# Performance work log

Hardware: AMD Instinct MI355X
Metric: run time of the kernel (lower is better)

## Reference

```python
import jax, jax.numpy as jnp
import numpy as np


def setup_inputs() -> dict:
    key = jax.random.key(0)
    k0, k1, k2, k3, k4 = jax.random.split(key, 5)
    feat0 = jax.random.normal(k0, (32, 256, 56, 56), dtype=jnp.float32)
    feat1 = jax.random.normal(k1, (32, 512, 28, 28), dtype=jnp.float32)
    feat2 = jax.random.normal(k2, (32, 1024, 14, 14), dtype=jnp.float32)
    feat3 = jax.random.normal(k3, (32, 2048, 7, 7), dtype=jnp.float32)
    # Conv2d(3840 -> 1024, kernel_size=1, bias=False): weight [emb, C_total]
    conv_w = jax.random.normal(k4, (1024, 3840), dtype=jnp.float32) * 0.02
    return {"feat0": feat0, "feat1": feat1, "feat2": feat2, "feat3": feat3, "conv_w": conv_w}


def reference(feat0, feat1, feat2, feat3, conv_w):
    # Target spatial size = earliest (largest) level.
    Ht, Wt = feat0.shape[2], feat0.shape[3]

    def up_mean(f):
        # Bilinear upsample (torch Upsample align_corners=False == jax 'bilinear'
        # half-pixel resize), then spatial mean per channel.  Because the 1x1
        # conv and global avg-pool are linear, pooling each upsampled level
        # first and applying the conv on the pooled vector is exactly the
        # same math as conv(concat(upsampled)) followed by avg-pool.
        B, C = f.shape[0], f.shape[1]
        up = jax.image.resize(f, (B, C, Ht, Wt), method='bilinear')  # [B,C,Ht,Wt]
        return jnp.mean(up, axis=(2, 3))  # [B,C]

    v = jnp.concatenate([up_mean(f) for f in (feat0, feat1, feat2, feat3)], axis=1)  # [B, 3840]
    # 1x1 conv (no bias) on pooled vector == GEMM with conv weight, then squeeze.
    return v @ conv_w.T  # [B, emb]
```

## Files before the change

### kernel.cpp

```cpp
#include <hip/hip_runtime.h>


__global__ __launch_bounds__(256) void pool_kernel(
    const float* __restrict__ f0, const float* __restrict__ f1,
    const float* __restrict__ f2, const float* __restrict__ f3,
    float* __restrict__ v)
{
    __shared__ float l[3136];
    int bid = blockIdx.x;
    int t = threadIdx.x;

    if (bid < 8192) {
        const float4* p = (const float4*)(f0 + (size_t)bid * 3136);
        float4 a = p[t], b2 = p[t + 256], c = p[t + 512];
        float s = a.x + a.y + a.z + a.w
                + b2.x + b2.y + b2.z + b2.w
                + c.x + c.y + c.z + c.w;
        if (t < 16) { float4 d = p[t + 768]; s += d.x + d.y + d.z + d.w; }
        #pragma unroll
        for (int o = 32; o; o >>= 1) s += __shfl_xor(s, o);
        if ((t & 63) == 0) l[t >> 6] = s;
        __syncthreads();
        if (t == 0)
            v[(bid >> 8) * 3840 + (bid & 255)] =
                (l[0] + l[1] + l[2] + l[3]) * (1.f / 3136.f);
        return;
    }

    float4* lf = (float4*)l;
    if (bid < 12288) {
        int blk = bid - 8192;
        const float4* src = (const float4*)(f1 + (size_t)blk * 3136);
        lf[t] = src[t]; lf[t + 256] = src[t + 256]; lf[t + 512] = src[t + 512];
        if (t < 16) lf[t + 768] = src[t + 768];
        __syncthreads();
        int w = t >> 6, lane = t & 63;
        const float* base = l + w * 784;
        float s = 0.f;
        #pragma unroll
        for (int i = 0; i < 12; ++i) s += base[lane + (i << 6)];
        if (lane < 16) s += base[768 + lane];
        #pragma unroll
        for (int o = 32; o; o >>= 1) s += __shfl_xor(s, o);
        if (lane == 0) {
            int q = blk * 4 + w;
            v[(q >> 9) * 3840 + 256 + (q & 511)] = s * (1.f / 784.f);
        }
    } else if (bid < 14336) {
        int blk = bid - 12288;
        const float4* src = (const float4*)(f2 + (size_t)blk * 3136);
        lf[t] = src[t]; lf[t + 256] = src[t + 256]; lf[t + 512] = src[t + 512];
        if (t < 16) lf[t + 768] = src[t + 768];
        __syncthreads();
        int p = t >> 4, j = t & 15;
        const float* base = l + p * 196;
        float s = 0.f;
        #pragma unroll
        for (int i = 0; i < 12; ++i) s += base[j + (i << 4)];
        if (j < 4) s += base[192 + j];
        s += __shfl_xor(s, 8); s += __shfl_xor(s, 4);
        s += __shfl_xor(s, 2); s += __shfl_xor(s, 1);
        if (j == 0) {
            int q = blk * 16 + p;
            v[(q >> 10) * 3840 + 768 + (q & 1023)] = s * (1.f / 196.f);
        }
    } else {
        int blk = bid - 14336;
        const float4* src = (const float4*)(f3 + (size_t)blk * 3136);
        lf[t] = src[t]; lf[t + 256] = src[t + 256]; lf[t + 512] = src[t + 512];
        if (t < 16) lf[t + 768] = src[t + 768];
        __syncthreads();
        int p = t >> 2, j = t & 3;
        const float* base = l + p * 49;
        float s = 0.f;
        #pragma unroll
        for (int i = 0; i < 12; ++i) s += base[j + (i << 2)];
        if (j == 0) s += base[48];
        s += __shfl_xor(s, 2); s += __shfl_xor(s, 1);
        if (j == 0) {
            int q = blk * 64 + p;
            v[(q >> 11) * 3840 + 1792 + (q & 2047)] = s * (1.f / 49.f);
        }
    }
}

#define KT 120

__global__ __launch_bounds__(256) void gemm_kernel(
    const float* __restrict__ v, const float* __restrict__ W,
    float* __restrict__ partials)
{
    __shared__ float vs[32][124];
    __shared__ float wsh[64][124];
    int t = threadIdx.x;
    int et = blockIdx.x & 15, ks = blockIdx.x >> 4;
    int e0 = et << 6, k0 = ks * KT;

    {
        int f = t;
        #pragma unroll
        for (int i = 0; i < 3; ++i, f += 256) {
            int row = f / 30, c4 = f % 30;
            *(float4*)&vs[row][c4 * 4] =
                *(const float4*)&v[row * 3840 + k0 + c4 * 4];
        }
        if (t < 192) {
            f = t + 768;
            int row = f / 30, c4 = f % 30;
            *(float4*)&vs[row][c4 * 4] =
                *(const float4*)&v[row * 3840 + k0 + c4 * 4];
        }
    }
    {
        int f = t;
        #pragma unroll
        for (int i = 0; i < 7; ++i, f += 256) {
            int row = f / 30, c4 = f % 30;
            *(float4*)&wsh[row][c4 * 4] =
                *(const float4*)&W[(size_t)(e0 + row) * 3840 + k0 + c4 * 4];
        }
        if (t < 128) {
            f = t + 1792;
            int row = f / 30, c4 = f % 30;
            *(float4*)&wsh[row][c4 * 4] =
                *(const float4*)&W[(size_t)(e0 + row) * 3840 + k0 + c4 * 4];
        }
    }
    __syncthreads();

    int bg = t >> 5, eg = t & 31;
    int b0 = bg << 2;
    float acc[4][2] = {};
    #pragma unroll 5
    for (int k = 0; k < KT; k += 4) {
        float4 vv[4], ww[2];
        #pragma unroll
        for (int i = 0; i < 4; ++i) vv[i] = *(const float4*)&vs[b0 + i][k];
        #pragma unroll
        for (int j = 0; j < 2; ++j) ww[j] = *(const float4*)&wsh[eg + (j << 5)][k];
        #pragma unroll
        for (int i = 0; i < 4; ++i)
            #pragma unroll
            for (int j = 0; j < 2; ++j)
                acc[i][j] += vv[i].x * ww[j].x + vv[i].y * ww[j].y +
                             vv[i].z * ww[j].z + vv[i].w * ww[j].w;
    }

    float* pout = partials + (size_t)ks * 32768 + (size_t)b0 * 1024 + e0 + eg;
    #pragma unroll
    for (int i = 0; i < 4; ++i)
        #pragma unroll
        for (int j = 0; j < 2; ++j)
            pout[i * 1024 + (j << 5)] = acc[i][j];
}

__global__ __launch_bounds__(256) void reduce_kernel(
    const float* __restrict__ partials, float* __restrict__ out)
{
    int idx = blockIdx.x * 256 + threadIdx.x;
    float s = 0.f;
    #pragma unroll
    for (int sp = 0; sp < 32; ++sp) s += partials[sp * 32768 + idx];
    out[idx] = s;
}

extern "C" void kernel_launch(void* const* d_in, const int* in_sizes, int n_in,
                              void* d_out, int out_size, void* d_ws, size_t ws_size,
                              hipStream_t stream)
{
    const float* f0 = (const float*)d_in[0];
    const float* f1 = (const float*)d_in[1];
    const float* f2 = (const float*)d_in[2];
    const float* f3 = (const float*)d_in[3];
    const float* W  = (const float*)d_in[4];
    float* out = (float*)d_out;

    float* v        = (float*)d_ws;
    float* partials = v + 32 * 3840;

    pool_kernel<<<15360, 256, 0, stream>>>(f0, f1, f2, f3, v);
    gemm_kernel<<<512, 256, 0, stream>>>(v, W, partials);
    reduce_kernel<<<128, 256, 0, stream>>>(partials, out);
}
```

Before: 233.7 us.

## Use direct global-to-LDS loads with larger pool blocks and unified segment sums

Rewrites the pooling kernel so each block loads 4 channel-groups of 3136 floats straight into LDS via global_load_lds. Every thread then sums one 49-element segment, followed by level-specific shuffle reductions. This cuts the grid from 15360 to 3840 blocks and avoids staging through registers. The GEMM staging now issues all global loads before the shared stores, and the reduce kernel uses four independent accumulators. The 50KB LDS footprint limits occupancy and may reduce memory-level parallelism.

```diff
diff --git a/kernel.cpp b/kernel.cpp
--- a/kernel.cpp
+++ b/kernel.cpp
@@ -1,86 +1,68 @@
 #include <hip/hip_runtime.h>
 
+
+#define AS1(p) ((const __attribute__((address_space(1))) void*)(p))
+#define AS3(p) ((__attribute__((address_space(3))) void*)(p))
 
 __global__ __launch_bounds__(256) void pool_kernel(
     const float* __restrict__ f0, const float* __restrict__ f1,
     const float* __restrict__ f2, const float* __restrict__ f3,
     float* __restrict__ v)
 {
-    __shared__ float l[3136];
-    int bid = blockIdx.x;
-    int t = threadIdx.x;
+    __shared__ float l[12544];
+    int bid = blockIdx.x, t = threadIdx.x;
+    int wave = t >> 6, lane = t & 63;
 
-    if (bid < 8192) {
-        const float4* p = (const float4*)(f0 + (size_t)bid * 3136);
-        float4 a = p[t], b2 = p[t + 256], c = p[t + 512];
-        float s = a.x + a.y + a.z + a.w
-                + b2.x + b2.y + b2.z + b2.w
-                + c.x + c.y + c.z + c.w;
-        if (t < 16) { float4 d = p[t + 768]; s += d.x + d.y + d.z + d.w; }
+    const float* base;
+    if (bid < 2048)      base = f0 + (size_t)bid * 12544;
+    else if (bid < 3072) base = f1 + (size_t)(bid - 2048) * 12544;
+    else if (bid < 3584) base = f2 + (size_t)(bid - 3072) * 12544;
+    else                 base = f3 + (size_t)(bid - 3584) * 12544;
+
+    {
+        const float* g = base + wave * 3136;
+        float* ld = l + wave * 3136;
         #pragma unroll
-        for (int o = 32; o; o >>= 1) s += __shfl_xor(s, o);
-        if ((t & 63) == 0) l[t >> 6] = s;
-        __syncthreads();
-        if (t == 0)
-            v[(bid >> 8) * 3840 + (bid & 255)] =
-                (l[0] + l[1] + l[2] + l[3]) * (1.f / 3136.f);
-        return;
+        for (int r = 0; r < 12; ++r) {
+            __builtin_amdgcn_global_load_lds(
+                AS1(g + r * 256 + lane * 4), AS3(ld + r * 256), 16, 0, 0);
+        }
+        if (lane < 16) {
+            __builtin_amdgcn_global_load_lds(
+                AS1(g + 3072 + lane * 4), AS3(ld + 3072), 16, 0, 0);
+        }
     }
+    asm volatile("s_waitcnt vmcnt(0)" ::: "memory");
+    __syncthreads();
 
-    float4* lf = (float4*)l;
-    if (bid < 12288) {
-        int blk = bid - 8192;
-        const float4* src = (const float4*)(f1 + (size_t)blk * 3136);
-        lf[t] = src[t]; lf[t + 256] = src[t + 256]; lf[t + 512] = src[t + 512];
-        if (t < 16) lf[t + 768] = src[t + 768];
-        __syncthreads();
-        int w = t >> 6, lane = t & 63;
-        const float* base = l + w * 784;
-        float s = 0.f;
-        #pragma unroll
-        for (int i = 0; i < 12; ++i) s += base[lane + (i << 6)];
-        if (lane < 16) s += base[768 + lane];
+    const float* seg = l + t * 49;
+    float s = 0.f;
+    #pragma unroll
+    for (int i = 0; i < 49; ++i) s += seg[i];
+
+    if (bid < 2048) {
         #pragma unroll
         for (int o = 32; o; o >>= 1) s += __shfl_xor(s, o);
         if (lane == 0) {
-            int q = blk * 4 + w;
+            int q = bid * 4 + wave;
+            v[(q >> 8) * 3840 + (q & 255)] = s * (1.f / 3136.f);
+        }
+    } else if (bid < 3072) {
+        s += __shfl_xor(s, 8); s += __shfl_xor(s, 4);
+        s += __shfl_xor(s, 2); s += __shfl_xor(s, 1);
+        if ((t & 15) == 0) {
+            int q = (bid - 2048) * 16 + (t >> 4);
             v[(q >> 9) * 3840 + 256 + (q & 511)] = s * (1.f / 784.f);
         }
-    } else if (bid < 14336) {
-        int blk = bid - 12288;
-        const float4* src = (const float4*)(f2 + (size_t)blk * 3136);
-        lf[t] = src[t]; lf[t + 256] = src[t + 256]; lf[t + 512] = src[t + 512];
-        if (t < 16) lf[t + 768] = src[t + 768];
-        __syncthreads();
-        int p = t >> 4, j = t & 15;
-        const float* base = l + p * 196;
-        float s = 0.f;
-        #pragma unroll
-        for (int i = 0; i < 12; ++i) s += base[j + (i << 4)];
-        if (j < 4) s += base[192 + j];
-        s += __shfl_xor(s, 8); s += __shfl_xor(s, 4);
+    } else if (bid < 3584) {
         s += __shfl_xor(s, 2); s += __shfl_xor(s, 1);
-        if (j == 0) {
-            int q = blk * 16 + p;
+        if ((t & 3) == 0) {
+            int q = (bid - 3072) * 64 + (t >> 2);
             v[(q >> 10) * 3840 + 768 + (q & 1023)] = s * (1.f / 196.f);
         }
     } else {
-        int blk = bid - 14336;
-        const float4* src = (const float4*)(f3 + (size_t)blk * 3136);
-        lf[t] = src[t]; lf[t + 256] = src[t + 256]; lf[t + 512] = src[t + 512];
-        if (t < 16) lf[t + 768] = src[t + 768];
-        __syncthreads();
-        int p = t >> 2, j = t & 3;
-        const float* base = l + p * 49;
-        float s = 0.f;
-        #pragma unroll
-        for (int i = 0; i < 12; ++i) s += base[j + (i << 2)];
-        if (j == 0) s += base[48];
-        s += __shfl_xor(s, 2); s += __shfl_xor(s, 1);
-        if (j == 0) {
-            int q = blk * 64 + p;
-            v[(q >> 11) * 3840 + 1792 + (q & 2047)] = s * (1.f / 49.f);
-        }
+        int q = (bid - 3584) * 256 + t;
+        v[(q >> 11) * 3840 + 1792 + (q & 2047)] = s * (1.f / 49.f);
     }
 }
 
@@ -97,34 +79,46 @@
     int e0 = et << 6, k0 = ks * KT;
 
     {
-        int f = t;
+        float4 tmp[7];
+        int row[7], c4[7];
         #pragma unroll
-        for (int i = 0; i < 3; ++i, f += 256) {
-            int row = f / 30, c4 = f % 30;
-            *(float4*)&vs[row][c4 * 4] =
-                *(const float4*)&v[row * 3840 + k0 + c4 * 4];
+        for (int i = 0; i < 7; ++i) {
+            int f = t + (i << 8);
+            row[i] = f / 30; c4[i] = f % 30;
+            tmp[i] = *(const float4*)&W[(size_t)(e0 + row[i]) * 3840 + k0 + c4[i] * 4];
         }
-        if (t < 192) {
-            f = t + 768;
-            int row = f / 30, c4 = f % 30;
-            *(float4*)&vs[row][c4 * 4] =
-                *(const float4*)&v[row * 3840 + k0 + c4 * 4];
+        float4 tail; int rowt = 0, c4t = 0;
+        if (t < 128) {
+            int f = t + 1792;
+            rowt = f / 30; c4t = f % 30;
+            tail = *(const float4*)&W[(size_t)(e0 + rowt) * 3840 + k0 + c4t * 4];
         }
+        #pragma unroll
+        for (int i = 0; i < 7; ++i)
+            *(float4*)&wsh[row[i]][c4[i] * 4] = tmp[i];
+        if (t < 128)
+            *(float4*)&wsh[rowt][c4t * 4] = tail;
     }
     {
-        int f = t;
+        float4 tmp[3];
+        int row[3], c4[3];
         #pragma unroll
-        for (int i = 0; i < 7; ++i, f += 256) {
-            int row = f / 30, c4 = f % 30;
-            *(float4*)&wsh[row][c4 * 4] =
-                *(const float4*)&W[(size_t)(e0 + row) * 3840 + k0 + c4 * 4];
+        for (int i = 0; i < 3; ++i) {
+            int f = t + (i << 8);
+            row[i] = f / 30; c4[i] = f % 30;
+            tmp[i] = *(const float4*)&v[row[i] * 3840 + k0 + c4[i] * 4];
         }
-        if (t < 128) {
-            f = t + 1792;
-            int row = f / 30, c4 = f % 30;
-            *(float4*)&wsh[row][c4 * 4] =
-                *(const float4*)&W[(size_t)(e0 + row) * 3840 + k0 + c4 * 4];
+        float4 tail; int rowt = 0, c4t = 0;
+        if (t < 192) {
+            int f = t + 768;
+            rowt = f / 30; c4t = f % 30;
+            tail = *(const float4*)&v[rowt * 3840 + k0 + c4t * 4];
         }
+        #pragma unroll
+        for (int i = 0; i < 3; ++i)
+            *(float4*)&vs[row[i]][c4[i] * 4] = tmp[i];
+        if (t < 192)
+            *(float4*)&vs[rowt][c4t * 4] = tail;
     }
     __syncthreads();
 
@@ -158,10 +152,15 @@
     const float* __restrict__ partials, float* __restrict__ out)
 {
     int idx = blockIdx.x * 256 + threadIdx.x;
-    float s = 0.f;
+    float s0 = 0.f, s1 = 0.f, s2 = 0.f, s3 = 0.f;
     #pragma unroll
-    for (int sp = 0; sp < 32; ++sp) s += partials[sp * 32768 + idx];
-    out[idx] = s;
+    for (int sp = 0; sp < 32; sp += 4) {
+        s0 += partials[(sp + 0) * 32768 + idx];
+        s1 += partials[(sp + 1) * 32768 + idx];
+        s2 += partials[(sp + 2) * 32768 + idx];
+        s3 += partials[(sp + 3) * 32768 + idx];
+    }
+    out[idx] = (s0 + s1) + (s2 + s3);
 }
 
 extern "C" void kernel_launch(void* const* d_in, const int* in_sizes, int n_in,
@@ -178,7 +177,7 @@
     float* v        = (float*)d_ws;
     float* partials = v + 32 * 3840;
 
-    pool_kernel<<<15360, 256, 0, stream>>>(f0, f1, f2, f3, v);
+    pool_kernel<<<3840, 256, 0, stream>>>(f0, f1, f2, f3, v);
     gemm_kernel<<<512, 256, 0, stream>>>(v, W, partials);
     reduce_kernel<<<128, 256, 0, stream>>>(partials, out);
 }
```

New measurement: 233.9 us. No clear change (+0.0%).
